# Kernel tuning notes

Measured on AMD Instinct MI355X. Metric: run time of the kernel, lower is better.

Reference implementation:

```python
import jax, jax.numpy as jnp
import numpy as np

B, S, H, NREL = 4, 512, 256, 99


def setup_inputs() -> dict:
    key = jax.random.key(0)
    ks = jax.random.split(key, 6)
    return {
        "queries": jax.random.normal(ks[0], (B, S, H), dtype=jnp.float32),
        "keys": jax.random.normal(ks[1], (B, S, H), dtype=jnp.float32),
        "relations": jax.random.randint(ks[2], (B, S, S), 0, NREL, dtype=jnp.int64),
        "Wq": jax.random.normal(ks[3], (H, H), dtype=jnp.float32) * 0.02,
        "bq": jnp.zeros((H,), dtype=jnp.float32),
        "Wk": jax.random.normal(ks[4], (H, H), dtype=jnp.float32) * 0.02,
        "bk": jnp.zeros((H,), dtype=jnp.float32),
        "rel_emb": jax.random.normal(ks[5], (NREL, H), dtype=jnp.float32) * 0.02,
    }


def reference(queries, keys, relations, Wq, bq, Wk, bk, rel_emb):
    # Linear projections (torch Linear: x @ W.T + b)
    q = queries @ Wq.T + bq        # [B, Sq, H]
    k = keys @ Wk.T + bk           # [B, Sk, H]
    r = rel_emb[relations]         # [B, Sq, Sk, H]

    # single head: qk^T + q . r^T, scaled
    qk = jnp.einsum("bqd,bkd->bqk", q, k)       # [B, Sq, Sk]
    qr = jnp.einsum("bqd,bqkd->bqk", q, r)      # [B, Sq, Sk]
    scale = 1.0 / jnp.sqrt(jnp.asarray(q.shape[-1], q.dtype))
    logits = (qk + qr) * scale
    return jax.nn.softmax(logits, axis=-1)       # squeezed head dim -> [B, Sq, Sk]
```

## Files before the change

### kernel.cpp

```cpp
#include <hip/hip_runtime.h>

typedef __attribute__((ext_vector_type(8))) short bf8;
typedef __attribute__((ext_vector_type(4))) float f4;

#define QBF  0
#define KBF  524288
#define REBF 1048576

static __device__ __forceinline__ short bfr(float x) {
    union { float f; unsigned u; } v; v.f = x;
    return (short)((v.u + 0x7FFF + ((v.u >> 16) & 1)) >> 16);
}
static __device__ __forceinline__ bf8 pack8(float4 a, float4 b) {
    bf8 r;
    r[0] = bfr(a.x); r[1] = bfr(a.y); r[2] = bfr(a.z); r[3] = bfr(a.w);
    r[4] = bfr(b.x); r[5] = bfr(b.y); r[6] = bfr(b.z); r[7] = bfr(b.w);
    return r;
}

__global__ __launch_bounds__(512) void proj_kernel(const float* __restrict__ queries,
                                                   const float* __restrict__ keys,
                                                   const float* __restrict__ bq,
                                                   const float* __restrict__ bk,
                                                   const float* __restrict__ Wq,
                                                   const float* __restrict__ Wk,
                                                   const float* __restrict__ rel_emb,
                                                   short* __restrict__ ws) {
    __shared__ short w_l[64 * 264];
    int blk = blockIdx.x;
    int tid = threadIdx.x;

    if (blk >= 256) {
        int g = (blk - 256) * 512 + tid;
        if (g < 1792) {
            int idx = g * 16;
            float4 a = make_float4(0.f, 0.f, 0.f, 0.f), b = a, c = a, d = a;
            if ((idx >> 8) < 99) {
                const float4* s = (const float4*)(rel_emb + idx);
                a = s[0]; b = s[1]; c = s[2]; d = s[3];
            }
            *(bf8*)(ws + REBF + idx) = pack8(a, b);
            *(bf8*)(ws + REBF + idx + 8) = pack8(c, d);
        }
        return;
    }

    int mat = blk >> 7;
    int t = blk & 127;
    int m0 = (t >> 2) * 64;
    int n0 = (t & 3) * 64;
    const float* x = mat ? keys : queries;
    const float* W = mat ? Wk : Wq;
    const float* bias = mat ? bk : bq;
    short* outp = ws + (mat ? KBF : QBF);

    int w = tid >> 6;
    int lane = tid & 63;
    int n15 = lane & 15, quad = lane >> 4;
    int wr = w & 3, wc = w >> 2;

#pragma unroll
    for (int cc = 0; cc < 4; cc++) {
        int chunk = cc * 512 + tid;
        int row = chunk >> 5, col8 = chunk & 31;
        const float4* s = (const float4*)(W + (n0 + row) * 256 + col8 * 8);
        *(bf8*)&w_l[row * 264 + col8 * 8] = pack8(s[0], s[1]);
    }

    int mrow = m0 + wr * 16 + n15;
    bf8 afr[8];
#pragma unroll
    for (int kk = 0; kk < 8; kk++) {
        const float4* ap = (const float4*)(x + mrow * 256 + kk * 32 + quad * 8);
        afr[kk] = pack8(ap[0], ap[1]);
    }
    __syncthreads();

    f4 z = {0.f, 0.f, 0.f, 0.f};
    f4 c[2] = {z, z};
#pragma unroll
    for (int nt = 0; nt < 2; nt++) {
        const short* wrp = &w_l[(wc * 32 + nt * 16 + n15) * 264 + quad * 8];
#pragma unroll
        for (int kk = 0; kk < 8; kk++) {
            bf8 bfrag = *(const bf8*)(wrp + kk * 32);
            c[nt] = __builtin_amdgcn_mfma_f32_16x16x32_bf16(afr[kk], bfrag, c[nt], 0, 0, 0);
        }
    }

    int mbase = m0 + wr * 16 + quad * 4;
#pragma unroll
    for (int nt = 0; nt < 2; nt++) {
        int col = n0 + wc * 32 + nt * 16 + n15;
        float bv = bias[col];
#pragma unroll
        for (int reg = 0; reg < 4; reg++)
            outp[(mbase + reg) * 256 + col] = bfr(c[nt][reg] + bv);
    }
}

__global__ __launch_bounds__(512) void attn_kernel(const int* __restrict__ relations,
                                                   const short* __restrict__ ws,
                                                   float* __restrict__ out) {
    __shared__ float qr_l[16][112];
    __shared__ float red_m[16][8];
    __shared__ float red_s[16][8];

    int blk = blockIdx.x;
    int b = blk >> 6;
    int i0 = (blk & 63) * 8;
    int gi0 = b * 512 + i0;
    int w = threadIdx.x >> 6;
    int lane = threadIdx.x & 63;
    int n15 = lane & 15, quad = lane >> 4;
    int j0 = w * 64;

    const int* rb = relations + (gi0 + (quad & 1) * 4) * 512 + j0 + n15;
    int rv[4][4];
#pragma unroll
    for (int reg = 0; reg < 4; reg++)
#pragma unroll
        for (int nt = 0; nt < 4; nt++)
            rv[nt][reg] = rb[reg * 512 + nt * 16];

    const short* qbf = ws + QBF;
    const short* kbf = ws + KBF;
    const short* rebf = ws + REBF;

    int arow = gi0 + (n15 & 7);
    bf8 afr[8];
#pragma unroll
    for (int kk = 0; kk < 8; kk++)
        afr[kk] = *(const bf8*)(qbf + arow * 256 + kk * 32 + quad * 8);

    f4 z = {0.f, 0.f, 0.f, 0.f};
    f4 c[4] = {z, z, z, z};
#pragma unroll
    for (int nt = 0; nt < 4; nt++) {
        int krow = b * 512 + j0 + nt * 16 + n15;
        const short* kr = kbf + krow * 256 + quad * 8;
#pragma unroll
        for (int kk = 0; kk < 8; kk++) {
            bf8 bfrag = *(const bf8*)(kr + kk * 32);
            c[nt] = __builtin_amdgcn_mfma_f32_16x16x32_bf16(afr[kk], bfrag, c[nt], 0, 0, 0);
        }
    }

    if (w < 7) {
        f4 cq = z;
        const short* rr = rebf + (w * 16 + n15) * 256 + quad * 8;
#pragma unroll
        for (int kk = 0; kk < 8; kk++) {
            bf8 bfrag = *(const bf8*)(rr + kk * 32);
            cq = __builtin_amdgcn_mfma_f32_16x16x32_bf16(afr[kk], bfrag, cq, 0, 0, 0);
        }
#pragma unroll
        for (int reg = 0; reg < 4; reg++)
            qr_l[quad * 4 + reg][w * 16 + n15] = cq[reg];
    }
    __syncthreads();

    const float scale = 0.0625f;
    float lg[4][4];
#pragma unroll
    for (int nt = 0; nt < 4; nt++)
#pragma unroll
        for (int reg = 0; reg < 4; reg++)
            lg[nt][reg] = (c[nt][reg] + qr_l[quad * 4 + reg][rv[nt][reg]]) * scale;

    float pm[4];
#pragma unroll
    for (int reg = 0; reg < 4; reg++) {
        float m = fmaxf(fmaxf(lg[0][reg], lg[1][reg]), fmaxf(lg[2][reg], lg[3][reg]));
#pragma unroll
        for (int d = 1; d <= 8; d <<= 1) m = fmaxf(m, __shfl_xor(m, d, 64));
        pm[reg] = m;
    }
    if (n15 == 0)
#pragma unroll
        for (int reg = 0; reg < 4; reg++) red_m[quad * 4 + reg][w] = pm[reg];
    __syncthreads();
    float M[4];
#pragma unroll
    for (int reg = 0; reg < 4; reg++) {
        f4 a0 = *(const f4*)&red_m[quad * 4 + reg][0];
        f4 a1 = *(const f4*)&red_m[quad * 4 + reg][4];
        M[reg] = fmaxf(fmaxf(fmaxf(a0[0], a0[1]), fmaxf(a0[2], a0[3])),
                       fmaxf(fmaxf(a1[0], a1[1]), fmaxf(a1[2], a1[3])));
    }

    float ps[4];
#pragma unroll
    for (int reg = 0; reg < 4; reg++) {
        float s = 0.f;
#pragma unroll
        for (int nt = 0; nt < 4; nt++) {
            float e = __expf(lg[nt][reg] - M[reg]);
            lg[nt][reg] = e;
            s += e;
        }
#pragma unroll
        for (int d = 1; d <= 8; d <<= 1) s += __shfl_xor(s, d, 64);
        ps[reg] = s;
    }
    if (n15 == 0)
#pragma unroll
        for (int reg = 0; reg < 4; reg++) red_s[quad * 4 + reg][w] = ps[reg];
    __syncthreads();
    float inv[4];
#pragma unroll
    for (int reg = 0; reg < 4; reg++) {
        f4 a0 = *(const f4*)&red_s[quad * 4 + reg][0];
        f4 a1 = *(const f4*)&red_s[quad * 4 + reg][4];
        inv[reg] = 1.f / (a0[0] + a0[1] + a0[2] + a0[3] + a1[0] + a1[1] + a1[2] + a1[3]);
    }

    if (quad < 2) {
        float* ob = out + (gi0 + quad * 4) * 512 + j0 + n15;
#pragma unroll
        for (int reg = 0; reg < 4; reg++)
#pragma unroll
            for (int nt = 0; nt < 4; nt++)
                ob[reg * 512 + nt * 16] = lg[nt][reg] * inv[reg];
    }
}

extern "C" void kernel_launch(void* const* d_in, const int* in_sizes, int n_in,
                              void* d_out, int out_size, void* d_ws, size_t ws_size,
                              hipStream_t stream) {
    const float* queries = (const float*)d_in[0];
    const float* keys = (const float*)d_in[1];
    const int* relations = (const int*)d_in[2];
    const float* Wq = (const float*)d_in[3];
    const float* bq = (const float*)d_in[4];
    const float* Wk = (const float*)d_in[5];
    const float* bk = (const float*)d_in[6];
    const float* rel_emb = (const float*)d_in[7];
    short* wss = (short*)d_ws;
    float* out = (float*)d_out;

    hipLaunchKernelGGL(proj_kernel, dim3(260), dim3(512), 0, stream,
                       queries, keys, bq, bk, Wq, Wk, rel_emb, wss);
    hipLaunchKernelGGL(attn_kernel, dim3(256), dim3(512), 0, stream, relations, wss, out);
}
```

Before: 93.57 us.

## Fuse projections into attention kernel by reassociating q·Wk into keys

Removes the separate projection kernel and the bf16 workspace. Each attention block computes its 8 projected query rows, then forms t = q·Wk. That lets qk be computed as t·keys^T directly from raw keys, with the q·bk term added as a per-row scalar. This saves one launch and the global round trip, but every block now reads Wq, Wk (strided, element by element), keys and rel_emb as fp32 and converts them to bf16 again. It also adds two more dependent MFMA phases per block.

```diff
diff --git a/kernel.cpp b/kernel.cpp
--- a/kernel.cpp
+++ b/kernel.cpp
@@ -2,14 +2,14 @@
 
 typedef __attribute__((ext_vector_type(8))) short bf8;
 typedef __attribute__((ext_vector_type(4))) float f4;
-
-#define QBF  0
-#define KBF  524288
-#define REBF 1048576
 
 static __device__ __forceinline__ short bfr(float x) {
     union { float f; unsigned u; } v; v.f = x;
     return (short)((v.u + 0x7FFF + ((v.u >> 16) & 1)) >> 16);
+}
+static __device__ __forceinline__ float bf2f(short s) {
+    union { float f; unsigned u; } v; v.u = ((unsigned)(unsigned short)s) << 16;
+    return v.f;
 }
 static __device__ __forceinline__ bf8 pack8(float4 a, float4 b) {
     bf8 r;
@@ -18,93 +18,19 @@
     return r;
 }
 
-__global__ __launch_bounds__(512) void proj_kernel(const float* __restrict__ queries,
-                                                   const float* __restrict__ keys,
-                                                   const float* __restrict__ bq,
-                                                   const float* __restrict__ bk,
-                                                   const float* __restrict__ Wq,
-                                                   const float* __restrict__ Wk,
-                                                   const float* __restrict__ rel_emb,
-                                                   short* __restrict__ ws) {
-    __shared__ short w_l[64 * 264];
-    int blk = blockIdx.x;
-    int tid = threadIdx.x;
-
-    if (blk >= 256) {
-        int g = (blk - 256) * 512 + tid;
-        if (g < 1792) {
-            int idx = g * 16;
-            float4 a = make_float4(0.f, 0.f, 0.f, 0.f), b = a, c = a, d = a;
-            if ((idx >> 8) < 99) {
-                const float4* s = (const float4*)(rel_emb + idx);
-                a = s[0]; b = s[1]; c = s[2]; d = s[3];
-            }
-            *(bf8*)(ws + REBF + idx) = pack8(a, b);
-            *(bf8*)(ws + REBF + idx + 8) = pack8(c, d);
-        }
-        return;
-    }
-
-    int mat = blk >> 7;
-    int t = blk & 127;
-    int m0 = (t >> 2) * 64;
-    int n0 = (t & 3) * 64;
-    const float* x = mat ? keys : queries;
-    const float* W = mat ? Wk : Wq;
-    const float* bias = mat ? bk : bq;
-    short* outp = ws + (mat ? KBF : QBF);
-
-    int w = tid >> 6;
-    int lane = tid & 63;
-    int n15 = lane & 15, quad = lane >> 4;
-    int wr = w & 3, wc = w >> 2;
-
-#pragma unroll
-    for (int cc = 0; cc < 4; cc++) {
-        int chunk = cc * 512 + tid;
-        int row = chunk >> 5, col8 = chunk & 31;
-        const float4* s = (const float4*)(W + (n0 + row) * 256 + col8 * 8);
-        *(bf8*)&w_l[row * 264 + col8 * 8] = pack8(s[0], s[1]);
-    }
-
-    int mrow = m0 + wr * 16 + n15;
-    bf8 afr[8];
-#pragma unroll
-    for (int kk = 0; kk < 8; kk++) {
-        const float4* ap = (const float4*)(x + mrow * 256 + kk * 32 + quad * 8);
-        afr[kk] = pack8(ap[0], ap[1]);
-    }
-    __syncthreads();
-
-    f4 z = {0.f, 0.f, 0.f, 0.f};
-    f4 c[2] = {z, z};
-#pragma unroll
-    for (int nt = 0; nt < 2; nt++) {
-        const short* wrp = &w_l[(wc * 32 + nt * 16 + n15) * 264 + quad * 8];
-#pragma unroll
-        for (int kk = 0; kk < 8; kk++) {
-            bf8 bfrag = *(const bf8*)(wrp + kk * 32);
-            c[nt] = __builtin_amdgcn_mfma_f32_16x16x32_bf16(afr[kk], bfrag, c[nt], 0, 0, 0);
-        }
-    }
-
-    int mbase = m0 + wr * 16 + quad * 4;
-#pragma unroll
-    for (int nt = 0; nt < 2; nt++) {
-        int col = n0 + wc * 32 + nt * 16 + n15;
-        float bv = bias[col];
-#pragma unroll
-        for (int reg = 0; reg < 4; reg++)
-            outp[(mbase + reg) * 256 + col] = bfr(c[nt][reg] + bv);
-    }
-}
-
-__global__ __launch_bounds__(512) void attn_kernel(const int* __restrict__ relations,
-                                                   const short* __restrict__ ws,
-                                                   float* __restrict__ out) {
+__global__ __launch_bounds__(512) void fused_attn(
+    const float* __restrict__ queries, const float* __restrict__ keys,
+    const int* __restrict__ relations, const float* __restrict__ Wq,
+    const float* __restrict__ bq, const float* __restrict__ Wk,
+    const float* __restrict__ bk, const float* __restrict__ rel_emb,
+    float* __restrict__ out)
+{
+    __shared__ short q_l[8][264];
+    __shared__ short t_l[8][264];
     __shared__ float qr_l[16][112];
     __shared__ float red_m[16][8];
     __shared__ float red_s[16][8];
+    __shared__ float qbk_l[8];
 
     int blk = blockIdx.x;
     int b = blk >> 6;
@@ -113,9 +39,8 @@
     int w = threadIdx.x >> 6;
     int lane = threadIdx.x & 63;
     int n15 = lane & 15, quad = lane >> 4;
-    int j0 = w * 64;
-
-    const int* rb = relations + (gi0 + (quad & 1) * 4) * 512 + j0 + n15;
+
+    const int* rb = relations + (gi0 + (quad & 1) * 4) * 512 + w * 64 + n15;
     int rv[4][4];
 #pragma unroll
     for (int reg = 0; reg < 4; reg++)
@@ -123,40 +48,115 @@
         for (int nt = 0; nt < 4; nt++)
             rv[nt][reg] = rb[reg * 512 + nt * 16];
 
-    const short* qbf = ws + QBF;
-    const short* kbf = ws + KBF;
-    const short* rebf = ws + REBF;
+    f4 z = {0.f, 0.f, 0.f, 0.f};
 
     int arow = gi0 + (n15 & 7);
-    bf8 afr[8];
+    bf8 aq[8];
+#pragma unroll
+    for (int kk = 0; kk < 8; kk++) {
+        const float4* ap = (const float4*)(queries + arow * 256 + kk * 32 + quad * 8);
+        aq[kk] = pack8(ap[0], ap[1]);
+    }
+    {
+        f4 cq[2] = {z, z};
+#pragma unroll
+        for (int nt = 0; nt < 2; nt++) {
+            int col = w * 32 + nt * 16 + n15;
+            const float* wqr = Wq + col * 256 + quad * 8;
+#pragma unroll
+            for (int kk = 0; kk < 8; kk++) {
+                const float4* bp = (const float4*)(wqr + kk * 32);
+                cq[nt] = __builtin_amdgcn_mfma_f32_16x16x32_bf16(aq[kk], pack8(bp[0], bp[1]),
+                                                                 cq[nt], 0, 0, 0);
+            }
+        }
+        if (quad < 2) {
+#pragma unroll
+            for (int nt = 0; nt < 2; nt++) {
+                int col = w * 32 + nt * 16 + n15;
+                float bv = bq[col];
+#pragma unroll
+                for (int reg = 0; reg < 4; reg++)
+                    q_l[quad * 4 + reg][col] = bfr(cq[nt][reg] + bv);
+            }
+        }
+    }
+    __syncthreads();
+
+    bf8 aQ[8];
 #pragma unroll
     for (int kk = 0; kk < 8; kk++)
-        afr[kk] = *(const bf8*)(qbf + arow * 256 + kk * 32 + quad * 8);
-
-    f4 z = {0.f, 0.f, 0.f, 0.f};
+        aQ[kk] = *(const bf8*)&q_l[n15 & 7][kk * 32 + quad * 8];
+
+    {
+        f4 ct[2] = {z, z};
+#pragma unroll
+        for (int nt = 0; nt < 2; nt++) {
+            int h = w * 32 + nt * 16 + n15;
+#pragma unroll
+            for (int kk = 0; kk < 8; kk++) {
+                const float* wp = Wk + (kk * 32 + quad * 8) * 256 + h;
+                bf8 bf_;
+#pragma unroll
+                for (int j = 0; j < 8; j++) bf_[j] = bfr(wp[j * 256]);
+                ct[nt] = __builtin_amdgcn_mfma_f32_16x16x32_bf16(aQ[kk], bf_, ct[nt], 0, 0, 0);
+            }
+        }
+        if (quad < 2) {
+#pragma unroll
+            for (int nt = 0; nt < 2; nt++) {
+                int h = w * 32 + nt * 16 + n15;
+#pragma unroll
+                for (int reg = 0; reg < 4; reg++)
+                    t_l[quad * 4 + reg][h] = bfr(ct[nt][reg]);
+            }
+        }
+    }
+
+    {
+        const short* qp = &q_l[w][lane * 4];
+        float4 bkv = *(const float4*)(bk + lane * 4);
+        float a0 = bf2f(qp[0]) * bkv.x + bf2f(qp[1]) * bkv.y +
+                   bf2f(qp[2]) * bkv.z + bf2f(qp[3]) * bkv.w;
+#pragma unroll
+        for (int d = 1; d <= 32; d <<= 1) a0 += __shfl_xor(a0, d, 64);
+        if (lane == 0) qbk_l[w] = a0;
+    }
+    __syncthreads();
+
+    bf8 aT[8];
+#pragma unroll
+    for (int kk = 0; kk < 8; kk++)
+        aT[kk] = *(const bf8*)&t_l[n15 & 7][kk * 32 + quad * 8];
+
     f4 c[4] = {z, z, z, z};
 #pragma unroll
     for (int nt = 0; nt < 4; nt++) {
-        int krow = b * 512 + j0 + nt * 16 + n15;
-        const short* kr = kbf + krow * 256 + quad * 8;
+        int krow = b * 512 + w * 64 + nt * 16 + n15;
+        const float* kr = keys + krow * 256 + quad * 8;
 #pragma unroll
         for (int kk = 0; kk < 8; kk++) {
-            bf8 bfrag = *(const bf8*)(kr + kk * 32);
-            c[nt] = __builtin_amdgcn_mfma_f32_16x16x32_bf16(afr[kk], bfrag, c[nt], 0, 0, 0);
+            const float4* kp = (const float4*)(kr + kk * 32);
+            c[nt] = __builtin_amdgcn_mfma_f32_16x16x32_bf16(aT[kk], pack8(kp[0], kp[1]),
+                                                            c[nt], 0, 0, 0);
         }
     }
 
     if (w < 7) {
-        f4 cq = z;
-        const short* rr = rebf + (w * 16 + n15) * 256 + quad * 8;
+        f4 cr = z;
+        int rrow = w * 16 + n15;
+        bool valid = rrow < 99;
+        const float* rp = rel_emb + (valid ? rrow : 0) * 256 + quad * 8;
 #pragma unroll
         for (int kk = 0; kk < 8; kk++) {
-            bf8 bfrag = *(const bf8*)(rr + kk * 32);
-            cq = __builtin_amdgcn_mfma_f32_16x16x32_bf16(afr[kk], bfrag, cq, 0, 0, 0);
+            const float4* rpp = (const float4*)(rp + kk * 32);
+            float4 x0 = rpp[0], x1 = rpp[1];
+            if (!valid) { x0 = make_float4(0.f, 0.f, 0.f, 0.f); x1 = x0; }
+            cr = __builtin_amdgcn_mfma_f32_16x16x32_bf16(aQ[kk], pack8(x0, x1), cr, 0, 0, 0);
         }
 #pragma unroll
         for (int reg = 0; reg < 4; reg++)
-            qr_l[quad * 4 + reg][w * 16 + n15] = cq[reg];
+            qr_l[quad * 4 + reg][rrow] = cr[reg];
     }
     __syncthreads();
 
@@ -166,7 +166,8 @@
     for (int nt = 0; nt < 4; nt++)
 #pragma unroll
         for (int reg = 0; reg < 4; reg++)
-            lg[nt][reg] = (c[nt][reg] + qr_l[quad * 4 + reg][rv[nt][reg]]) * scale;
+            lg[nt][reg] = (c[nt][reg] + qr_l[quad * 4 + reg][rv[nt][reg]] +
+                           qbk_l[(quad & 1) * 4 + reg]) * scale;
 
     float pm[4];
 #pragma unroll
@@ -216,7 +217,7 @@
     }
 
     if (quad < 2) {
-        float* ob = out + (gi0 + quad * 4) * 512 + j0 + n15;
+        float* ob = out + (gi0 + quad * 4) * 512 + w * 64 + n15;
 #pragma unroll
         for (int reg = 0; reg < 4; reg++)
 #pragma unroll
@@ -236,10 +237,8 @@
     const float* Wk = (const float*)d_in[5];
     const float* bk = (const float*)d_in[6];
     const float* rel_emb = (const float*)d_in[7];
-    short* wss = (short*)d_ws;
     float* out = (float*)d_out;
 
-    hipLaunchKernelGGL(proj_kernel, dim3(260), dim3(512), 0, stream,
-                       queries, keys, bq, bk, Wq, Wk, rel_emb, wss);
-    hipLaunchKernelGGL(attn_kernel, dim3(256), dim3(512), 0, stream, relations, wss, out);
-}
+    hipLaunchKernelGGL(fused_attn, dim3(256), dim3(512), 0, stream,
+                       queries, keys, relations, Wq, bq, Wk, bk, rel_emb, out);
+}
```

Measured after the change: 107.6 us. +15.0%, slower.
